# Kernel tuning notes

Hardware: AMD Instinct MI355X
Metric: run time of the kernel (lower is better)

Reference implementation:

```python
import jax, jax.numpy as jnp
import numpy as np

B, T, D, H = 8, 4096, 512, 64

def setup_inputs() -> dict:
    key = jax.random.key(0)
    ks = jax.random.split(key, 6)
    s = 0.02  # small init scale so exp(K), exp(wbias) stay numerically tame
    return {
        "x": jax.random.normal(ks[0], (B, T, D), dtype=jnp.float32),
        "wq": jax.random.normal(ks[1], (H, D), dtype=jnp.float32) * s,
        "bq": jnp.zeros((H,), dtype=jnp.float32),
        "wk": jax.random.normal(ks[2], (H, D), dtype=jnp.float32) * s,
        "bk": jnp.zeros((H,), dtype=jnp.float32),
        "wv": jax.random.normal(ks[3], (H, D), dtype=jnp.float32) * s,
        "bv": jnp.zeros((H,), dtype=jnp.float32),
        "wp": jax.random.normal(ks[4], (D, H), dtype=jnp.float32) * s,
        "bp": jnp.zeros((D,), dtype=jnp.float32),
        "wbias": jax.random.normal(ks[5], (T, T), dtype=jnp.float32) * s,
    }

def reference(x, wq, bq, wk, bk, wv, bv, wp, bp, wbias):
    # Q, K, V projections: [B, T, H]
    Q = jnp.einsum('btd,hd->bth', x, wq) + bq
    K = jnp.einsum('btd,hd->bth', x, wk) + bk
    V = jnp.einsum('btd,hd->bth', x, wv) + bv
    ew = jnp.exp(wbias)              # [T, T], computed once
    eK = jnp.exp(K)                  # [B, T, H]
    num = jnp.einsum('ts,bsh->bth', ew, eK * V)
    den = jnp.einsum('ts,bsh->bth', ew, eK)
    Yt = jax.nn.sigmoid(Q) * (num / den)
    # output projection back to dim: [B, T, D]
    return jnp.einsum('bth,dh->btd', Yt, wp) + bp
```

## Files before the change

kernel.cpp:

```cpp
#include <hip/hip_runtime.h>
#include <math.h>

typedef _Float16 f16;
typedef __attribute__((ext_vector_type(8))) _Float16 f16x8;
typedef __attribute__((ext_vector_type(4))) _Float16 f16x4;
typedef __attribute__((ext_vector_type(4))) float f32x4;
typedef __attribute__((ext_vector_type(16))) float f32x16;

#define MFMA16(a, b, c) __builtin_amdgcn_mfma_f32_16x16x32_f16((a), (b), (c), 0, 0, 0)
#define MFMA32(a, b, c) __builtin_amdgcn_mfma_f32_32x32x16_f16((a), (b), (c), 0, 0, 0)

__device__ __forceinline__ void gld16(const f16* g, f16* l) {
  __builtin_amdgcn_global_load_lds(
      (const __attribute__((address_space(1))) unsigned int*)g,
      (__attribute__((address_space(3))) unsigned int*)l, 16, 0, 0);
}

__device__ __forceinline__ f16x8 pack8(const float* src) {
  float4 f0 = *(const float4*)src;
  float4 f1 = *(const float4*)(src + 4);
  f16x8 v;
  v[0] = (f16)f0.x; v[1] = (f16)f0.y; v[2] = (f16)f0.z; v[3] = (f16)f0.w;
  v[4] = (f16)f1.x; v[5] = (f16)f1.y; v[6] = (f16)f1.z; v[7] = (f16)f1.w;
  return v;
}

__global__ __launch_bounds__(256) void prep_ew(const float* __restrict__ wb,
                                               f16* __restrict__ ew) {
  const size_t stride = (size_t)gridDim.x * 256;
  const size_t total = (size_t)4096 * 4096 / 4;
  for (size_t i = (size_t)blockIdx.x * 256 + threadIdx.x; i < total; i += stride) {
    float4 f = ((const float4*)wb)[i];
    f16x4 o;
    o.x = (f16)expf(f.x); o.y = (f16)expf(f.y);
    o.z = (f16)expf(f.z); o.w = (f16)expf(f.w);
    ((f16x4*)ew)[i] = o;
  }
}

__global__ __launch_bounds__(256) void prep_w(const float* __restrict__ wq,
                                              const float* __restrict__ wk,
                                              const float* __restrict__ wv,
                                              const float* __restrict__ wp,
                                              f16* __restrict__ wqkvb,
                                              f16* __restrict__ wpb) {
  int i = blockIdx.x * 256 + threadIdx.x;
  wqkvb[i] = (f16)wk[i];
  wqkvb[32768 + i] = (f16)wv[i];
  wqkvb[65536 + i] = (f16)wq[i];
  wpb[i] = (f16)wp[i];
}

__global__ __launch_bounds__(256) void k1_qkv(const float* __restrict__ x,
                                              const f16* __restrict__ wqkvb,
                                              const float* __restrict__ bq,
                                              const float* __restrict__ bk,
                                              const float* __restrict__ bv,
                                              f16* __restrict__ sigQ,
                                              f16* __restrict__ XT) {
  __shared__ alignas(16) f16 sW[192 * 64];
  __shared__ alignas(16) f16 sX[64 * 64];
  const int tid = threadIdx.x;
  const int wave = tid >> 6, lane = tid & 63;
  const int m0 = blockIdx.x * 64;
  const int l15 = lane & 15;

  f32x4 accQ[4], accK[4], accV[4];
#pragma unroll
  for (int j = 0; j < 4; ++j) {
    accQ[j] = (f32x4){0.f, 0.f, 0.f, 0.f};
    accK[j] = (f32x4){0.f, 0.f, 0.f, 0.f};
    accV[j] = (f32x4){0.f, 0.f, 0.f, 0.f};
  }

  const int sc8 = tid & 7;
  const int wr8 = (tid >> 3) & 7;
  const int wcol = (sc8 ^ wr8) * 8;

  for (int ks = 0; ks < 512; ks += 64) {
#pragma unroll
    for (int q = 0; q < 6; ++q) {
      int r = q * 32 + (tid >> 3);
      gld16(wqkvb + (size_t)r * 512 + ks + wcol, &sW[r * 64 + sc8 * 8]);
    }
#pragma unroll
    for (int u = 0; u < 2; ++u) {
      int un = tid + u * 256;
      int r = un >> 3, c8 = un & 7;
      *(f16x8*)&sX[r * 64 + ((c8 ^ (r & 7)) * 8)] =
          pack8(x + (size_t)(m0 + r) * 512 + ks + c8 * 8);
    }
    __syncthreads();
#pragma unroll
    for (int kk = 0; kk < 2; ++kk) {
      const int c = kk * 4 + (lane >> 4);
      const int rK = wave * 16 + l15;
      const int rV = 64 + rK;
      f16x8 aK = *(const f16x8*)&sW[rK * 64 + ((c ^ (rK & 7)) * 8)];
      f16x8 aV = *(const f16x8*)&sW[rV * 64 + ((c ^ (rV & 7)) * 8)];
      f16x8 aQ = *(const f16x8*)&sX[rK * 64 + ((c ^ (rK & 7)) * 8)];
#pragma unroll
      for (int j = 0; j < 4; ++j) {
        const int rX = j * 16 + l15;
        const int rWq = 128 + j * 16 + l15;
        f16x8 bx = *(const f16x8*)&sX[rX * 64 + ((c ^ (rX & 7)) * 8)];
        f16x8 bw = *(const f16x8*)&sW[rWq * 64 + ((c ^ (rWq & 7)) * 8)];
        accK[j] = MFMA16(aK, bx, accK[j]);
        accV[j] = MFMA16(aV, bx, accV[j]);
        accQ[j] = MFMA16(aQ, bw, accQ[j]);
      }
    }
    __syncthreads();
  }
  const int b = m0 >> 12, t0 = m0 & 4095;
#pragma unroll
  for (int j = 0; j < 4; ++j) {
    const int h = j * 16 + l15;
    const float bqv = bq[h];
#pragma unroll
    for (int r = 0; r < 4; ++r) {
      const int m = m0 + wave * 16 + (lane >> 4) * 4 + r;
      const float v = accQ[j][r] + bqv;
      sigQ[(size_t)m * 64 + h] = (f16)(1.f / (1.f + expf(-v)));
    }
  }
#pragma unroll
  for (int r = 0; r < 4; ++r) {
    const int h = wave * 16 + (lane >> 4) * 4 + r;
    const float bkv = bk[h], bvv = bv[h];
    const size_t rowKV = (size_t)(b * 128 + h) * 4096;
    const size_t rowK = (size_t)(b * 128 + 64 + h) * 4096;
#pragma unroll
    for (int j = 0; j < 4; ++j) {
      const int t = t0 + j * 16 + l15;
      const float ek = expf(accK[j][r] + bkv);
      const float ev = accV[j][r] + bvv;
      XT[rowKV + t] = (f16)(ek * ev);
      XT[rowK + t] = (f16)ek;
    }
  }
}

__global__ __launch_bounds__(512, 2) void k2_big(const f16* __restrict__ A,
                                                 const f16* __restrict__ Bm,
                                                 const f16* __restrict__ sigQ,
                                                 f16* __restrict__ Yt) {
  __shared__ alignas(16) f16 smem[4][128 * 128];
  const int tid = threadIdx.x;
  const int wave = tid >> 6, lane = tid & 63;
  const int kq = wave >> 1;
  const int ws = wave & 1;
  const int bid = blockIdx.x;
  const int b = (bid >> 3) & 7;
  const int m0 = ((bid & 7) + 8 * (bid >> 6)) * 128;
  const f16* Bbase = Bm + (size_t)(b * 128) * 4096;

  const int srow = tid >> 4;
  const int sc16 = tid & 15;
  const int gcol = (sc16 ^ (srow & 15)) * 8;

  f32x16 acc[4][2];
#pragma unroll
  for (int i = 0; i < 4; ++i)
#pragma unroll
    for (int j = 0; j < 2; ++j)
#pragma unroll
      for (int r = 0; r < 16; ++r) acc[i][j][r] = 0.f;

#define K2_STAGE(buf, ks)                                                          \
  do {                                                                             \
    _Pragma("unroll") for (int q = 0; q < 4; ++q) {                                \
      int r = q * 32 + srow;                                                       \
      gld16(A + (size_t)(m0 + r) * 4096 + (ks) + gcol,                             \
            &smem[buf][r * 128 + sc16 * 8]);                                       \
      gld16(Bbase + (size_t)r * 4096 + (ks) + gcol,                                \
            &smem[2 + (buf)][r * 128 + sc16 * 8]);                                 \
    }                                                                              \
  } while (0)

  K2_STAGE(0, 0);
  K2_STAGE(1, 128);
  asm volatile("s_waitcnt vmcnt(8)" ::: "memory");
  __builtin_amdgcn_s_barrier();
  asm volatile("" ::: "memory");

  const int l31 = lane & 31, l15 = lane & 15, lhi = lane >> 5;
  const int c0 = kq * 4 + lhi;
  const int cx0 = (c0 ^ l15) * 8;
  const int cx1 = ((c0 + 2) ^ l15) * 8;
  const int nk = 4096 / 128;
  for (int t = 0; t < nk; ++t) {
    const int buf = t & 1;
    const f16* pA = smem[buf];
    const f16* pB = smem[2 + buf];
    f16x8 a0[4], a1[4], b0[2], b1[2];
#pragma unroll
    for (int i = 0; i < 4; ++i) a0[i] = *(const f16x8*)&pA[(i * 32 + l31) * 128 + cx0];
#pragma unroll
    for (int j = 0; j < 2; ++j)
      b0[j] = *(const f16x8*)&pB[(j * 64 + ws * 32 + l31) * 128 + cx0];
#pragma unroll
    for (int i = 0; i < 4; ++i) a1[i] = *(const f16x8*)&pA[(i * 32 + l31) * 128 + cx1];
#pragma unroll
    for (int j = 0; j < 2; ++j)
      b1[j] = *(const f16x8*)&pB[(j * 64 + ws * 32 + l31) * 128 + cx1];
    __builtin_amdgcn_s_setprio(1);
#pragma unroll
    for (int i = 0; i < 4; ++i)
#pragma unroll
      for (int j = 0; j < 2; ++j) acc[i][j] = MFMA32(a0[i], b0[j], acc[i][j]);
#pragma unroll
    for (int i = 0; i < 4; ++i)
#pragma unroll
      for (int j = 0; j < 2; ++j) acc[i][j] = MFMA32(a1[i], b1[j], acc[i][j]);
    __builtin_amdgcn_s_setprio(0);
    if (t + 1 < nk) {
      asm volatile("s_waitcnt lgkmcnt(0)" ::: "memory");
      __builtin_amdgcn_s_barrier();
      asm volatile("" ::: "memory");
      if (t + 2 < nk) {
        K2_STAGE(buf, (t + 2) * 128);
        asm volatile("s_waitcnt vmcnt(8)" ::: "memory");
      } else {
        asm volatile("s_waitcnt vmcnt(0)" ::: "memory");
      }
      __builtin_amdgcn_s_barrier();
      asm volatile("" ::: "memory");
    }
  }
#undef K2_STAGE

  __syncthreads();
  float* scr = (float*)smem;
  const int rit0 = 4 * lhi;
#define MRG_ADDR(reg, i, j, r) \
  ((reg) * 16384 + ((i) * 32 + ((r) & 3) + 8 * ((r) >> 2) + rit0) * 128 + (j) * 64 + ws * 32 + l31)
  if (kq & 1) {
#pragma unroll
    for (int i = 0; i < 4; ++i)
#pragma unroll
      for (int j = 0; j < 2; ++j)
#pragma unroll
        for (int r = 0; r < 16; ++r) scr[MRG_ADDR(kq >> 1, i, j, r)] = acc[i][j][r];
  }
  __syncthreads();
  if (!(kq & 1)) {
#pragma unroll
    for (int i = 0; i < 4; ++i)
#pragma unroll
      for (int j = 0; j < 2; ++j)
#pragma unroll
        for (int r = 0; r < 16; ++r) acc[i][j][r] += scr[MRG_ADDR(kq >> 1, i, j, r)];
  }
  __syncthreads();
  if (kq == 2) {
#pragma unroll
    for (int i = 0; i < 4; ++i)
#pragma unroll
      for (int j = 0; j < 2; ++j)
#pragma unroll
        for (int r = 0; r < 16; ++r) scr[MRG_ADDR(0, i, j, r)] = acc[i][j][r];
  }
  __syncthreads();
  if (kq == 0) {
#pragma unroll
    for (int i = 0; i < 4; ++i)
#pragma unroll
      for (int j = 0; j < 2; ++j)
#pragma unroll
        for (int r = 0; r < 16; ++r) acc[i][j][r] += scr[MRG_ADDR(0, i, j, r)];
    const int h = ws * 32 + l31;
#pragma unroll
    for (int i = 0; i < 4; ++i)
#pragma unroll
      for (int r = 0; r < 16; ++r) {
        const int trow = m0 + i * 32 + (r & 3) + 8 * (r >> 2) + rit0;
        const size_t mrow = (size_t)b * 4096 + trow;
        const float sq = (float)sigQ[mrow * 64 + h];
        Yt[mrow * 64 + h] = (f16)(sq * acc[i][0][r] / acc[i][1][r]);
      }
  }
#undef MRG_ADDR
}

__global__ __launch_bounds__(256) void k4_out(const f16* __restrict__ Yt,
                                              const f16* __restrict__ wpb,
                                              const float* __restrict__ bp,
                                              float* __restrict__ out) {
  __shared__ alignas(16) f16 sA[128 * 64];
  __shared__ alignas(16) f16 sB[128 * 64];
  const int tid = threadIdx.x;
  const int wave = tid >> 6, lane = tid & 63;
  const int m0 = blockIdx.x * 128;
  const int n0 = blockIdx.y * 128;
  const int wm = (wave >> 1) * 64;
  const int wn = (wave & 1) * 64;
  const int l15 = lane & 15;
  const int sc8 = tid & 7;
  const int scol = (sc8 ^ ((tid >> 3) & 7)) * 8;

#pragma unroll
  for (int q = 0; q < 4; ++q) {
    int r = q * 32 + (tid >> 3);
    gld16(Yt + (size_t)(m0 + r) * 64 + scol, &sA[r * 64 + sc8 * 8]);
    gld16(wpb + (size_t)(n0 + r) * 64 + scol, &sB[r * 64 + sc8 * 8]);
  }
  __syncthreads();

  f32x4 acc[4][4];
#pragma unroll
  for (int i = 0; i < 4; ++i)
#pragma unroll
    for (int j = 0; j < 4; ++j) acc[i][j] = (f32x4){0.f, 0.f, 0.f, 0.f};

#pragma unroll
  for (int kk = 0; kk < 2; ++kk) {
    const int c = kk * 4 + (lane >> 4);
    f16x8 af[4], bfr[4];
#pragma unroll
    for (int i = 0; i < 4; ++i) {
      const int r = wm + i * 16 + l15;
      af[i] = *(const f16x8*)&sA[r * 64 + ((c ^ (r & 7)) * 8)];
    }
#pragma unroll
    for (int j = 0; j < 4; ++j) {
      const int r = wn + j * 16 + l15;
      bfr[j] = *(const f16x8*)&sB[r * 64 + ((c ^ (r & 7)) * 8)];
    }
#pragma unroll
    for (int i = 0; i < 4; ++i)
#pragma unroll
      for (int j = 0; j < 4; ++j) acc[i][j] = MFMA16(af[i], bfr[j], acc[i][j]);
  }

#pragma unroll
  for (int i = 0; i < 4; ++i) {
    const int row = m0 + wm + i * 16 + (lane >> 4) * 4;
#pragma unroll
    for (int j = 0; j < 4; ++j) {
      const int col = n0 + wn + j * 16 + l15;
      const float bpv = bp[col];
#pragma unroll
      for (int r = 0; r < 4; ++r)
        out[(size_t)(row + r) * 512 + col] = acc[i][j][r] + bpv;
    }
  }
}

extern "C" void kernel_launch(void* const* d_in, const int* in_sizes, int n_in,
                              void* d_out, int out_size, void* d_ws, size_t ws_size,
                              hipStream_t stream) {
  const float* x = (const float*)d_in[0];
  const float* wq = (const float*)d_in[1];
  const float* bq = (const float*)d_in[2];
  const float* wk = (const float*)d_in[3];
  const float* bk = (const float*)d_in[4];
  const float* wv = (const float*)d_in[5];
  const float* bv = (const float*)d_in[6];
  const float* wp = (const float*)d_in[7];
  const float* bp = (const float*)d_in[8];
  const float* wbias = (const float*)d_in[9];
  float* out = (float*)d_out;

  char* ws = (char*)d_ws;
  f16* ew = (f16*)(ws);
  f16* XT = (f16*)(ws + 33554432);
  f16* sigQ = (f16*)(ws + 41943040);
  f16* Yt = (f16*)(ws + 46137344);
  f16* wqkvb = (f16*)(ws + 50331648);
  f16* wpb = (f16*)(ws + 50528256);

  prep_ew<<<4096, 256, 0, stream>>>(wbias, ew);
  prep_w<<<128, 256, 0, stream>>>(wq, wk, wv, wp, wqkvb, wpb);
  k1_qkv<<<512, 256, 0, stream>>>(x, wqkvb, bq, bk, bv, sigQ, XT);
  k2_big<<<256, 512, 0, stream>>>(ew, XT, sigQ, Yt);
  k4_out<<<dim3(256, 4), 256, 0, stream>>>(Yt, wpb, bp, out);
}
```

Baseline: 99.63 us.

## Switch k2 to triple-buffered 64-wide K stages with single barrier per step

The main big GEMM kernel now uses a 3-stage ring of 64-column K tiles (96KB LDS) instead of double-buffered 128-column tiles (128KB). The next-next stage is issued at the start of each iteration, so there is one barrier per step instead of two. The cross-wave reduction is serialized to fit the smaller scratch area. Dropping the occupancy hint of 2 blocks per CU and halving K per step doubles the loop trips and barriers, which may reduce MFMA density per sync.

Result: no change. 99.33 us (-0.3%).

```diff
diff --git a/kernel.cpp b/kernel.cpp
--- a/kernel.cpp
+++ b/kernel.cpp
@@ -141,11 +141,11 @@
   }
 }
 
-__global__ __launch_bounds__(512, 2) void k2_big(const f16* __restrict__ A,
-                                                 const f16* __restrict__ Bm,
-                                                 const f16* __restrict__ sigQ,
-                                                 f16* __restrict__ Yt) {
-  __shared__ alignas(16) f16 smem[4][128 * 128];
+__global__ __launch_bounds__(512) void k2_big(const f16* __restrict__ A,
+                                              const f16* __restrict__ Bm,
+                                              const f16* __restrict__ sigQ,
+                                              f16* __restrict__ Yt) {
+  __shared__ alignas(16) f16 smem[3 * 16384];
   const int tid = threadIdx.x;
   const int wave = tid >> 6, lane = tid & 63;
   const int kq = wave >> 1;
@@ -153,11 +153,12 @@
   const int bid = blockIdx.x;
   const int b = (bid >> 3) & 7;
   const int m0 = ((bid & 7) + 8 * (bid >> 6)) * 128;
-  const f16* Bbase = Bm + (size_t)(b * 128) * 4096;
-
-  const int srow = tid >> 4;
-  const int sc16 = tid & 15;
-  const int gcol = (sc16 ^ (srow & 15)) * 8;
+  const f16* Bb = Bm + (size_t)(b * 128) * 4096;
+
+  const int srow8 = tid >> 3;
+  const int sc8 = tid & 7;
+  const int gsw = (sc8 ^ (srow8 & 7)) * 8;
+  const int dlin = srow8 * 64 + sc8 * 8;
 
   f32x16 acc[4][2];
 #pragma unroll
@@ -167,90 +168,88 @@
 #pragma unroll
       for (int r = 0; r < 16; ++r) acc[i][j][r] = 0.f;
 
-#define K2_STAGE(buf, ks)                                                          \
-  do {                                                                             \
-    _Pragma("unroll") for (int q = 0; q < 4; ++q) {                                \
-      int r = q * 32 + srow;                                                       \
-      gld16(A + (size_t)(m0 + r) * 4096 + (ks) + gcol,                             \
-            &smem[buf][r * 128 + sc16 * 8]);                                       \
-      gld16(Bbase + (size_t)r * 4096 + (ks) + gcol,                                \
-            &smem[2 + (buf)][r * 128 + sc16 * 8]);                                 \
-    }                                                                              \
+#define K2_STAGE(bb, ks)                                                         \
+  do {                                                                           \
+    gld16(A + (size_t)(m0 + srow8) * 4096 + (ks) + gsw, &smem[(bb) + dlin]);     \
+    gld16(A + (size_t)(m0 + 64 + srow8) * 4096 + (ks) + gsw,                     \
+          &smem[(bb) + 4096 + dlin]);                                            \
+    gld16(Bb + (size_t)srow8 * 4096 + (ks) + gsw, &smem[(bb) + 8192 + dlin]);    \
+    gld16(Bb + (size_t)(64 + srow8) * 4096 + (ks) + gsw,                         \
+          &smem[(bb) + 12288 + dlin]);                                           \
   } while (0)
 
   K2_STAGE(0, 0);
-  K2_STAGE(1, 128);
-  asm volatile("s_waitcnt vmcnt(8)" ::: "memory");
+  K2_STAGE(16384, 64);
+  asm volatile("s_waitcnt vmcnt(4)" ::: "memory");
+  __builtin_amdgcn_sched_barrier(0);
   __builtin_amdgcn_s_barrier();
-  asm volatile("" ::: "memory");
-
-  const int l31 = lane & 31, l15 = lane & 15, lhi = lane >> 5;
-  const int c0 = kq * 4 + lhi;
-  const int cx0 = (c0 ^ l15) * 8;
-  const int cx1 = ((c0 + 2) ^ l15) * 8;
-  const int nk = 4096 / 128;
+
+  const int l31 = lane & 31, lhi = lane >> 5;
+  const int cx = ((kq * 2 + lhi) ^ (lane & 7)) * 8;
+  const int nk = 64;
+  int bb = 0;
   for (int t = 0; t < nk; ++t) {
-    const int buf = t & 1;
-    const f16* pA = smem[buf];
-    const f16* pB = smem[2 + buf];
-    f16x8 a0[4], a1[4], b0[2], b1[2];
-#pragma unroll
-    for (int i = 0; i < 4; ++i) a0[i] = *(const f16x8*)&pA[(i * 32 + l31) * 128 + cx0];
+    int bb2 = bb + 32768;
+    if (bb2 >= 49152) bb2 -= 49152;
+    if (t < nk - 2) K2_STAGE(bb2, (t + 2) * 64);
+    const f16* pA = &smem[bb];
+    const f16* pB = &smem[bb + 8192];
+    f16x8 af[4], bf2[2];
+#pragma unroll
+    for (int i = 0; i < 4; ++i) af[i] = *(const f16x8*)&pA[(i * 32 + l31) * 64 + cx];
 #pragma unroll
     for (int j = 0; j < 2; ++j)
-      b0[j] = *(const f16x8*)&pB[(j * 64 + ws * 32 + l31) * 128 + cx0];
-#pragma unroll
-    for (int i = 0; i < 4; ++i) a1[i] = *(const f16x8*)&pA[(i * 32 + l31) * 128 + cx1];
-#pragma unroll
-    for (int j = 0; j < 2; ++j)
-      b1[j] = *(const f16x8*)&pB[(j * 64 + ws * 32 + l31) * 128 + cx1];
+      bf2[j] = *(const f16x8*)&pB[(j * 64 + ws * 32 + l31) * 64 + cx];
+    asm volatile("s_waitcnt lgkmcnt(0)" ::: "memory");
+    __builtin_amdgcn_sched_barrier(0);
     __builtin_amdgcn_s_setprio(1);
 #pragma unroll
     for (int i = 0; i < 4; ++i)
 #pragma unroll
-      for (int j = 0; j < 2; ++j) acc[i][j] = MFMA32(a0[i], b0[j], acc[i][j]);
-#pragma unroll
-    for (int i = 0; i < 4; ++i)
-#pragma unroll
-      for (int j = 0; j < 2; ++j) acc[i][j] = MFMA32(a1[i], b1[j], acc[i][j]);
+      for (int j = 0; j < 2; ++j) acc[i][j] = MFMA32(af[i], bf2[j], acc[i][j]);
     __builtin_amdgcn_s_setprio(0);
-    if (t + 1 < nk) {
-      asm volatile("s_waitcnt lgkmcnt(0)" ::: "memory");
-      __builtin_amdgcn_s_barrier();
-      asm volatile("" ::: "memory");
-      if (t + 2 < nk) {
-        K2_STAGE(buf, (t + 2) * 128);
-        asm volatile("s_waitcnt vmcnt(8)" ::: "memory");
-      } else {
-        asm volatile("s_waitcnt vmcnt(0)" ::: "memory");
-      }
-      __builtin_amdgcn_s_barrier();
-      asm volatile("" ::: "memory");
-    }
+    if (t < nk - 2) {
+      asm volatile("s_waitcnt vmcnt(4)" ::: "memory");
+    } else {
+      asm volatile("s_waitcnt vmcnt(0)" ::: "memory");
+    }
+    __builtin_amdgcn_sched_barrier(0);
+    __builtin_amdgcn_s_barrier();
+    bb += 16384;
+    if (bb == 49152) bb = 0;
   }
 #undef K2_STAGE
 
   __syncthreads();
   float* scr = (float*)smem;
   const int rit0 = 4 * lhi;
-#define MRG_ADDR(reg, i, j, r) \
-  ((reg) * 16384 + ((i) * 32 + ((r) & 3) + 8 * ((r) >> 2) + rit0) * 128 + (j) * 64 + ws * 32 + l31)
-  if (kq & 1) {
-#pragma unroll
-    for (int i = 0; i < 4; ++i)
-#pragma unroll
-      for (int j = 0; j < 2; ++j)
-#pragma unroll
-        for (int r = 0; r < 16; ++r) scr[MRG_ADDR(kq >> 1, i, j, r)] = acc[i][j][r];
-  }
-  __syncthreads();
-  if (!(kq & 1)) {
-#pragma unroll
-    for (int i = 0; i < 4; ++i)
-#pragma unroll
-      for (int j = 0; j < 2; ++j)
-#pragma unroll
-        for (int r = 0; r < 16; ++r) acc[i][j][r] += scr[MRG_ADDR(kq >> 1, i, j, r)];
+#define MRG(i, j, r) \
+  (((i) * 32 + ((r) & 3) + 8 * ((r) >> 2) + rit0) * 128 + (j) * 64 + ws * 32 + l31)
+  if (kq == 1) {
+#pragma unroll
+    for (int i = 0; i < 4; ++i)
+#pragma unroll
+      for (int j = 0; j < 2; ++j)
+#pragma unroll
+        for (int r = 0; r < 16; ++r) scr[MRG(i, j, r)] = acc[i][j][r];
+  }
+  __syncthreads();
+  if (kq == 0) {
+#pragma unroll
+    for (int i = 0; i < 4; ++i)
+#pragma unroll
+      for (int j = 0; j < 2; ++j)
+#pragma unroll
+        for (int r = 0; r < 16; ++r) acc[i][j][r] += scr[MRG(i, j, r)];
+  }
+  __syncthreads();
+  if (kq == 3) {
+#pragma unroll
+    for (int i = 0; i < 4; ++i)
+#pragma unroll
+      for (int j = 0; j < 2; ++j)
+#pragma unroll
+        for (int r = 0; r < 16; ++r) scr[MRG(i, j, r)] = acc[i][j][r];
   }
   __syncthreads();
   if (kq == 2) {
@@ -259,7 +258,16 @@
 #pragma unroll
       for (int j = 0; j < 2; ++j)
 #pragma unroll
-        for (int r = 0; r < 16; ++r) scr[MRG_ADDR(0, i, j, r)] = acc[i][j][r];
+        for (int r = 0; r < 16; ++r) acc[i][j][r] += scr[MRG(i, j, r)];
+  }
+  __syncthreads();
+  if (kq == 2) {
+#pragma unroll
+    for (int i = 0; i < 4; ++i)
+#pragma unroll
+      for (int j = 0; j < 2; ++j)
+#pragma unroll
+        for (int r = 0; r < 16; ++r) scr[MRG(i, j, r)] = acc[i][j][r];
   }
   __syncthreads();
   if (kq == 0) {
@@ -268,7 +276,7 @@
 #pragma unroll
       for (int j = 0; j < 2; ++j)
 #pragma unroll
-        for (int r = 0; r < 16; ++r) acc[i][j][r] += scr[MRG_ADDR(0, i, j, r)];
+        for (int r = 0; r < 16; ++r) acc[i][j][r] += scr[MRG(i, j, r)];
     const int h = ws * 32 + l31;
 #pragma unroll
     for (int i = 0; i < 4; ++i)
@@ -280,7 +288,7 @@
         Yt[mrow * 64 + h] = (f16)(sq * acc[i][0][r] / acc[i][1][r]);
       }
   }
-#undef MRG_ADDR
+#undef MRG
 }
 
 __global__ __launch_bounds__(256) void k4_out(const f16* __restrict__ Yt,
```

## Stage A tiles through registers with deeper prefetch in k2_big main loop

Applied to the files above, without the earlier changes.

The A operand of the big time-mixing GEMM is now loaded from global memory into registers three tiles ahead and then written to LDS. B keeps using direct global-to-LDS loads two tiles ahead. The loop is manually unrolled with ping-pong register buffers and sched_barriers, and explicit per-iteration vmcnt waits are dropped. The min-blocks-per-CU hint is removed, so the compiler gets more registers for the extra prefetch buffers. This aims to hide global latency better, at the cost of more VGPRs and relying on implicit waitcnt ordering for the asynchronous B loads.

Result: slower. 106.1 us (+6.5%).

```diff
diff --git a/kernel.cpp b/kernel.cpp
--- a/kernel.cpp
+++ b/kernel.cpp
@@ -141,11 +141,11 @@
   }
 }
 
-__global__ __launch_bounds__(512, 2) void k2_big(const f16* __restrict__ A,
-                                                 const f16* __restrict__ Bm,
-                                                 const f16* __restrict__ sigQ,
-                                                 f16* __restrict__ Yt) {
-  __shared__ alignas(16) f16 smem[4][128 * 128];
+__global__ __launch_bounds__(512) void k2_big(const f16* __restrict__ A,
+                                              const f16* __restrict__ Bm,
+                                              const f16* __restrict__ sigQ,
+                                              f16* __restrict__ Yt) {
+  __shared__ alignas(16) f16 smem[4][16384];
   const int tid = threadIdx.x;
   const int wave = tid >> 6, lane = tid & 63;
   const int kq = wave >> 1;
@@ -153,12 +153,20 @@
   const int bid = blockIdx.x;
   const int b = (bid >> 3) & 7;
   const int m0 = ((bid & 7) + 8 * (bid >> 6)) * 128;
-  const f16* Bbase = Bm + (size_t)(b * 128) * 4096;
+  const f16* Bb = Bm + (size_t)(b * 128) * 4096;
 
   const int srow = tid >> 4;
   const int sc16 = tid & 15;
   const int gcol = (sc16 ^ (srow & 15)) * 8;
 
+  int aRow[4], aCol[4];
+#pragma unroll
+  for (int u = 0; u < 4; ++u) {
+    int d = u * 512 + tid;
+    aRow[u] = d >> 4;
+    aCol[u] = ((d & 15) ^ ((d >> 4) & 15)) * 8;
+  }
+
   f32x16 acc[4][2];
 #pragma unroll
   for (int i = 0; i < 4; ++i)
@@ -167,68 +175,107 @@
 #pragma unroll
       for (int r = 0; r < 16; ++r) acc[i][j][r] = 0.f;
 
-#define K2_STAGE(buf, ks)                                                          \
-  do {                                                                             \
-    _Pragma("unroll") for (int q = 0; q < 4; ++q) {                                \
-      int r = q * 32 + srow;                                                       \
-      gld16(A + (size_t)(m0 + r) * 4096 + (ks) + gcol,                             \
-            &smem[buf][r * 128 + sc16 * 8]);                                       \
-      gld16(Bbase + (size_t)r * 4096 + (ks) + gcol,                                \
-            &smem[2 + (buf)][r * 128 + sc16 * 8]);                                 \
-    }                                                                              \
-  } while (0)
-
-  K2_STAGE(0, 0);
-  K2_STAGE(1, 128);
-  asm volatile("s_waitcnt vmcnt(8)" ::: "memory");
-  __builtin_amdgcn_s_barrier();
-  asm volatile("" ::: "memory");
+  f16x8 arE[4], arO[4];
 
   const int l31 = lane & 31, l15 = lane & 15, lhi = lane >> 5;
   const int c0 = kq * 4 + lhi;
   const int cx0 = (c0 ^ l15) * 8;
   const int cx1 = ((c0 + 2) ^ l15) * 8;
-  const int nk = 4096 / 128;
-  for (int t = 0; t < nk; ++t) {
-    const int buf = t & 1;
-    const f16* pA = smem[buf];
-    const f16* pB = smem[2 + buf];
-    f16x8 a0[4], a1[4], b0[2], b1[2];
-#pragma unroll
-    for (int i = 0; i < 4; ++i) a0[i] = *(const f16x8*)&pA[(i * 32 + l31) * 128 + cx0];
-#pragma unroll
-    for (int j = 0; j < 2; ++j)
-      b0[j] = *(const f16x8*)&pB[(j * 64 + ws * 32 + l31) * 128 + cx0];
-#pragma unroll
-    for (int i = 0; i < 4; ++i) a1[i] = *(const f16x8*)&pA[(i * 32 + l31) * 128 + cx1];
-#pragma unroll
-    for (int j = 0; j < 2; ++j)
-      b1[j] = *(const f16x8*)&pB[(j * 64 + ws * 32 + l31) * 128 + cx1];
-    __builtin_amdgcn_s_setprio(1);
-#pragma unroll
-    for (int i = 0; i < 4; ++i)
-#pragma unroll
-      for (int j = 0; j < 2; ++j) acc[i][j] = MFMA32(a0[i], b0[j], acc[i][j]);
-#pragma unroll
-    for (int i = 0; i < 4; ++i)
-#pragma unroll
-      for (int j = 0; j < 2; ++j) acc[i][j] = MFMA32(a1[i], b1[j], acc[i][j]);
-    __builtin_amdgcn_s_setprio(0);
-    if (t + 1 < nk) {
-      asm volatile("s_waitcnt lgkmcnt(0)" ::: "memory");
-      __builtin_amdgcn_s_barrier();
-      asm volatile("" ::: "memory");
-      if (t + 2 < nk) {
-        K2_STAGE(buf, (t + 2) * 128);
-        asm volatile("s_waitcnt vmcnt(8)" ::: "memory");
-      } else {
-        asm volatile("s_waitcnt vmcnt(0)" ::: "memory");
-      }
-      __builtin_amdgcn_s_barrier();
-      asm volatile("" ::: "memory");
-    }
-  }
-#undef K2_STAGE
+
+#define SB0 __builtin_amdgcn_sched_barrier(0)
+
+#define K2_ALOAD(dst, T)                                                        \
+  do {                                                                          \
+    _Pragma("unroll") for (int u = 0; u < 4; ++u)                               \
+        dst[u] = *(const f16x8*)(A + (size_t)(m0 + aRow[u]) * 4096 +            \
+                                 (size_t)(T) * 128 + aCol[u]);                  \
+  } while (0)
+
+#define K2_AWRITE(c, src)                                                       \
+  do {                                                                          \
+    _Pragma("unroll") for (int u = 0; u < 4; ++u)                               \
+        *(f16x8*)&smem[c][(u * 512 + tid) * 8] = src[u];                        \
+  } while (0)
+
+#define K2_BSTAGE(c, T)                                                         \
+  do {                                                                          \
+    _Pragma("unroll") for (int q = 0; q < 4; ++q) {                             \
+      int r = q * 32 + srow;                                                    \
+      gld16(Bb + (size_t)r * 4096 + (size_t)(T) * 128 + gcol,                   \
+            &smem[2 + (c)][r * 128 + sc16 * 8]);                                \
+    }                                                                           \
+  } while (0)
+
+#define K2_COMPUTE(c)                                                           \
+  do {                                                                          \
+    const f16* pA = smem[c];                                                    \
+    const f16* pB = smem[2 + (c)];                                              \
+    f16x8 a0[4], a1[4], b0[2], b1[2];                                           \
+    _Pragma("unroll") for (int i = 0; i < 4; ++i)                               \
+        a0[i] = *(const f16x8*)&pA[(i * 32 + l31) * 128 + cx0];                 \
+    _Pragma("unroll") for (int j = 0; j < 2; ++j)                               \
+        b0[j] = *(const f16x8*)&pB[(j * 64 + ws * 32 + l31) * 128 + cx0];       \
+    _Pragma("unroll") for (int i = 0; i < 4; ++i)                               \
+        a1[i] = *(const f16x8*)&pA[(i * 32 + l31) * 128 + cx1];                 \
+    _Pragma("unroll") for (int j = 0; j < 2; ++j)                               \
+        b1[j] = *(const f16x8*)&pB[(j * 64 + ws * 32 + l31) * 128 + cx1];       \
+    __builtin_amdgcn_s_setprio(1);                                              \
+    _Pragma("unroll") for (int i = 0; i < 4; ++i)                               \
+        _Pragma("unroll") for (int j = 0; j < 2; ++j)                           \
+            acc[i][j] = MFMA32(a0[i], b0[j], acc[i][j]);                        \
+    _Pragma("unroll") for (int i = 0; i < 4; ++i)                               \
+        _Pragma("unroll") for (int j = 0; j < 2; ++j)                           \
+            acc[i][j] = MFMA32(a1[i], b1[j], acc[i][j]);                        \
+    __builtin_amdgcn_s_setprio(0);                                              \
+  } while (0)
+
+#define K2_BODY(T, CUR, NXT, DOLOAD)                                            \
+  do {                                                                          \
+    K2_COMPUTE((T) & 1);                                                        \
+    SB0;                                                                        \
+    __builtin_amdgcn_s_barrier();                                               \
+    SB0;                                                                        \
+    K2_AWRITE((T) & 1, CUR);   \
+    K2_BSTAGE((T) & 1, (T) + 2);                                                \
+    if (DOLOAD) K2_ALOAD(NXT, (T) + 3);                                         \
+    asm volatile("s_waitcnt lgkmcnt(0)" ::: "memory");                          \
+    SB0;                                                                        \
+    __builtin_amdgcn_s_barrier();                                               \
+    SB0;                                                                        \
+  } while (0)
+
+  K2_ALOAD(arE, 0);
+  K2_BSTAGE(0, 0);
+  K2_AWRITE(0, arE);
+  K2_ALOAD(arO, 1);
+  K2_BSTAGE(1, 1);
+  K2_AWRITE(1, arO);
+  K2_ALOAD(arE, 2);
+  asm volatile("s_waitcnt lgkmcnt(0)" ::: "memory");
+  SB0;
+  __builtin_amdgcn_s_barrier();
+  SB0;
+
+  for (int t = 0; t < 28; t += 2) {
+    K2_BODY(t, arE, arO, 1);
+    K2_BODY(t + 1, arO, arE, 1);
+  }
+  K2_BODY(28, arE, arO, 1);
+  K2_BODY(29, arO, arE, 0);
+  K2_COMPUTE(0);
+  SB0;
+  __builtin_amdgcn_s_barrier();
+  SB0;
+  asm volatile("s_waitcnt vmcnt(0)" ::: "memory");
+  SB0;
+  __builtin_amdgcn_s_barrier();
+  SB0;
+  K2_COMPUTE(1);
+#undef K2_BODY
+#undef K2_COMPUTE
+#undef K2_BSTAGE
+#undef K2_AWRITE
+#undef K2_ALOAD
 
   __syncthreads();
   float* scr = (float*)smem;
@@ -281,6 +328,7 @@
       }
   }
 #undef MRG_ADDR
+#undef SB0
 }
 
 __global__ __launch_bounds__(256) void k4_out(const f16* __restrict__ Yt,
```

## Fuse output projection into big GEMM kernel, widen to 1024 threads, merge prep kernels

Applied to the files above, without the earlier changes.

Merges the two prep kernels into one launch and fuses the output projection (Yt·Wp^T + bp) into the epilogue of the main exp(wbias)×XT GEMM, so Yt is never written to or read back from global memory. The main kernel moves to 1024-thread blocks, giving each of 16 waves a 2x2 tile of 32x32 MFMAs with a 4-way split-K reduced through LDS. It also switches to sched_barrier fencing. The trade-offs are lower occupancy (one block per CU), a heavier epilogue, and fewer MFMAs per wave per LDS load in the main loop.

Measured after the change: 95.66 us. -4.0%, faster.

```diff
diff --git a/kernel.cpp b/kernel.cpp
--- a/kernel.cpp
+++ b/kernel.cpp
@@ -25,8 +25,14 @@
   return v;
 }
 
-__global__ __launch_bounds__(256) void prep_ew(const float* __restrict__ wb,
-                                               f16* __restrict__ ew) {
+__global__ __launch_bounds__(256) void prep_ewpw(const float* __restrict__ wb,
+                                                 f16* __restrict__ ew,
+                                                 const float* __restrict__ wq,
+                                                 const float* __restrict__ wk,
+                                                 const float* __restrict__ wv,
+                                                 const float* __restrict__ wp,
+                                                 f16* __restrict__ wqkvb,
+                                                 f16* __restrict__ wpb) {
   const size_t stride = (size_t)gridDim.x * 256;
   const size_t total = (size_t)4096 * 4096 / 4;
   for (size_t i = (size_t)blockIdx.x * 256 + threadIdx.x; i < total; i += stride) {
@@ -36,19 +42,13 @@
     o.z = (f16)expf(f.z); o.w = (f16)expf(f.w);
     ((f16x4*)ew)[i] = o;
   }
-}
-
-__global__ __launch_bounds__(256) void prep_w(const float* __restrict__ wq,
-                                              const float* __restrict__ wk,
-                                              const float* __restrict__ wv,
-                                              const float* __restrict__ wp,
-                                              f16* __restrict__ wqkvb,
-                                              f16* __restrict__ wpb) {
-  int i = blockIdx.x * 256 + threadIdx.x;
-  wqkvb[i] = (f16)wk[i];
-  wqkvb[32768 + i] = (f16)wv[i];
-  wqkvb[65536 + i] = (f16)wq[i];
-  wpb[i] = (f16)wp[i];
+  if (blockIdx.x < 128) {
+    int i = blockIdx.x * 256 + threadIdx.x;
+    wqkvb[i] = (f16)wk[i];
+    wqkvb[32768 + i] = (f16)wv[i];
+    wqkvb[65536 + i] = (f16)wq[i];
+    wpb[i] = (f16)wp[i];
+  }
 }
 
 __global__ __launch_bounds__(256) void k1_qkv(const float* __restrict__ x,
@@ -141,210 +141,216 @@
   }
 }
 
-__global__ __launch_bounds__(512, 2) void k2_big(const f16* __restrict__ A,
-                                                 const f16* __restrict__ Bm,
-                                                 const f16* __restrict__ sigQ,
-                                                 f16* __restrict__ Yt) {
-  __shared__ alignas(16) f16 smem[4][128 * 128];
+__global__ __launch_bounds__(1024) void k2_big(const f16* __restrict__ A,
+                                               const f16* __restrict__ Bm,
+                                               const f16* __restrict__ sigQ,
+                                               const f16* __restrict__ wpb,
+                                               const float* __restrict__ bp,
+                                               float* __restrict__ out) {
+  __shared__ alignas(16) f16 smem[4][16384];
   const int tid = threadIdx.x;
-  const int wave = tid >> 6, lane = tid & 63;
-  const int kq = wave >> 1;
-  const int ws = wave & 1;
+  const int w = tid >> 6, lane = tid & 63;
+  const int kq = w >> 2;
+  const int wr = (w >> 1) & 1;
+  const int wc = w & 1;
   const int bid = blockIdx.x;
   const int b = (bid >> 3) & 7;
   const int m0 = ((bid & 7) + 8 * (bid >> 6)) * 128;
-  const f16* Bbase = Bm + (size_t)(b * 128) * 4096;
-
-  const int srow = tid >> 4;
-  const int sc16 = tid & 15;
-  const int gcol = (sc16 ^ (srow & 15)) * 8;
-
-  f32x16 acc[4][2];
-#pragma unroll
-  for (int i = 0; i < 4; ++i)
+  const f16* Bb = Bm + (size_t)(b * 128) * 4096;
+
+  int sRow[2], sCol[2];
+#pragma unroll
+  for (int u = 0; u < 2; ++u) {
+    int d = u * 1024 + tid;
+    sRow[u] = d >> 4;
+    sCol[u] = ((d & 15) ^ ((d >> 4) & 15)) * 8;
+  }
+
+  f32x16 acc[2][2];
+#pragma unroll
+  for (int i = 0; i < 2; ++i)
 #pragma unroll
     for (int j = 0; j < 2; ++j)
 #pragma unroll
       for (int r = 0; r < 16; ++r) acc[i][j][r] = 0.f;
 
-#define K2_STAGE(buf, ks)                                                          \
-  do {                                                                             \
-    _Pragma("unroll") for (int q = 0; q < 4; ++q) {                                \
-      int r = q * 32 + srow;                                                       \
-      gld16(A + (size_t)(m0 + r) * 4096 + (ks) + gcol,                             \
-            &smem[buf][r * 128 + sc16 * 8]);                                       \
-      gld16(Bbase + (size_t)r * 4096 + (ks) + gcol,                                \
-            &smem[2 + (buf)][r * 128 + sc16 * 8]);                                 \
-    }                                                                              \
+#define SB0 __builtin_amdgcn_sched_barrier(0)
+#define K2_STAGE(buf, ks)                                                       \
+  do {                                                                          \
+    _Pragma("unroll") for (int u = 0; u < 2; ++u) {                             \
+      gld16(A + (size_t)(m0 + sRow[u]) * 4096 + (ks) + sCol[u],                 \
+            &smem[buf][(u * 1024 + tid) * 8]);                                  \
+      gld16(Bb + (size_t)sRow[u] * 4096 + (ks) + sCol[u],                       \
+            &smem[2 + (buf)][(u * 1024 + tid) * 8]);                            \
+    }                                                                           \
   } while (0)
 
   K2_STAGE(0, 0);
   K2_STAGE(1, 128);
-  asm volatile("s_waitcnt vmcnt(8)" ::: "memory");
+  asm volatile("s_waitcnt vmcnt(4)" ::: "memory");
+  SB0;
   __builtin_amdgcn_s_barrier();
-  asm volatile("" ::: "memory");
+  SB0;
 
   const int l31 = lane & 31, l15 = lane & 15, lhi = lane >> 5;
   const int c0 = kq * 4 + lhi;
   const int cx0 = (c0 ^ l15) * 8;
   const int cx1 = ((c0 + 2) ^ l15) * 8;
-  const int nk = 4096 / 128;
+  const int arow0 = (wr * 64 + l31) * 128;
+  const int arow1 = (wr * 64 + 32 + l31) * 128;
+  const int brow0 = (wc * 32 + l31) * 128;
+  const int brow1 = (64 + wc * 32 + l31) * 128;
+
+  const int nk = 32;
   for (int t = 0; t < nk; ++t) {
-    const int buf = t & 1;
-    const f16* pA = smem[buf];
-    const f16* pB = smem[2 + buf];
-    f16x8 a0[4], a1[4], b0[2], b1[2];
-#pragma unroll
-    for (int i = 0; i < 4; ++i) a0[i] = *(const f16x8*)&pA[(i * 32 + l31) * 128 + cx0];
-#pragma unroll
-    for (int j = 0; j < 2; ++j)
-      b0[j] = *(const f16x8*)&pB[(j * 64 + ws * 32 + l31) * 128 + cx0];
-#pragma unroll
-    for (int i = 0; i < 4; ++i) a1[i] = *(const f16x8*)&pA[(i * 32 + l31) * 128 + cx1];
-#pragma unroll
-    for (int j = 0; j < 2; ++j)
-      b1[j] = *(const f16x8*)&pB[(j * 64 + ws * 32 + l31) * 128 + cx1];
+    const int cur = t & 1;
+    const f16* pA = smem[cur];
+    const f16* pB = smem[2 + cur];
+    f16x8 a00 = *(const f16x8*)&pA[arow0 + cx0];
+    f16x8 a10 = *(const f16x8*)&pA[arow1 + cx0];
+    f16x8 b00 = *(const f16x8*)&pB[brow0 + cx0];
+    f16x8 b10 = *(const f16x8*)&pB[brow1 + cx0];
+    f16x8 a01 = *(const f16x8*)&pA[arow0 + cx1];
+    f16x8 a11 = *(const f16x8*)&pA[arow1 + cx1];
+    f16x8 b01 = *(const f16x8*)&pB[brow0 + cx1];
+    f16x8 b11 = *(const f16x8*)&pB[brow1 + cx1];
     __builtin_amdgcn_s_setprio(1);
-#pragma unroll
-    for (int i = 0; i < 4; ++i)
-#pragma unroll
-      for (int j = 0; j < 2; ++j) acc[i][j] = MFMA32(a0[i], b0[j], acc[i][j]);
-#pragma unroll
-    for (int i = 0; i < 4; ++i)
-#pragma unroll
-      for (int j = 0; j < 2; ++j) acc[i][j] = MFMA32(a1[i], b1[j], acc[i][j]);
+    acc[0][0] = MFMA32(a00, b00, acc[0][0]);
+    acc[0][1] = MFMA32(a00, b10, acc[0][1]);
+    acc[1][0] = MFMA32(a10, b00, acc[1][0]);
+    acc[1][1] = MFMA32(a10, b10, acc[1][1]);
+    acc[0][0] = MFMA32(a01, b01, acc[0][0]);
+    acc[0][1] = MFMA32(a01, b11, acc[0][1]);
+    acc[1][0] = MFMA32(a11, b01, acc[1][0]);
+    acc[1][1] = MFMA32(a11, b11, acc[1][1]);
     __builtin_amdgcn_s_setprio(0);
-    if (t + 1 < nk) {
-      asm volatile("s_waitcnt lgkmcnt(0)" ::: "memory");
-      __builtin_amdgcn_s_barrier();
-      asm volatile("" ::: "memory");
-      if (t + 2 < nk) {
-        K2_STAGE(buf, (t + 2) * 128);
-        asm volatile("s_waitcnt vmcnt(8)" ::: "memory");
-      } else {
-        asm volatile("s_waitcnt vmcnt(0)" ::: "memory");
+    asm volatile("s_waitcnt lgkmcnt(0)" ::: "memory");
+    SB0;
+    __builtin_amdgcn_s_barrier();
+    SB0;
+    if (t + 2 < nk) {
+      K2_STAGE(cur, (t + 2) * 128);
+      asm volatile("s_waitcnt vmcnt(4)" ::: "memory");
+    } else {
+      asm volatile("s_waitcnt vmcnt(0)" ::: "memory");
+    }
+    SB0;
+    __builtin_amdgcn_s_barrier();
+    SB0;
+  }
+#undef K2_STAGE
+
+  f16x8 wpr[4];
+#pragma unroll
+  for (int u = 0; u < 4; ++u)
+    wpr[u] = *(const f16x8*)(wpb + (size_t)(u * 1024 + tid) * 8);
+
+  __syncthreads();
+  float* scr = (float*)smem;
+#define MADDR(reg, i, j, r) \
+  ((reg) * 16384 + (((wr * 2 + wc) * 4 + (i) * 2 + (j)) << 10) + ((r) << 6) + lane)
+  if (kq == 1) {
+#pragma unroll
+    for (int i = 0; i < 2; ++i)
+#pragma unroll
+      for (int j = 0; j < 2; ++j)
+#pragma unroll
+        for (int r = 0; r < 16; ++r) scr[MADDR(0, i, j, r)] = acc[i][j][r];
+  }
+  if (kq == 3) {
+#pragma unroll
+    for (int i = 0; i < 2; ++i)
+#pragma unroll
+      for (int j = 0; j < 2; ++j)
+#pragma unroll
+        for (int r = 0; r < 16; ++r) scr[MADDR(1, i, j, r)] = acc[i][j][r];
+  }
+  __syncthreads();
+  if (kq == 0) {
+#pragma unroll
+    for (int i = 0; i < 2; ++i)
+#pragma unroll
+      for (int j = 0; j < 2; ++j)
+#pragma unroll
+        for (int r = 0; r < 16; ++r) acc[i][j][r] += scr[MADDR(0, i, j, r)];
+  }
+  if (kq == 2) {
+#pragma unroll
+    for (int i = 0; i < 2; ++i)
+#pragma unroll
+      for (int j = 0; j < 2; ++j)
+#pragma unroll
+        for (int r = 0; r < 16; ++r) acc[i][j][r] += scr[MADDR(1, i, j, r)];
+  }
+  __syncthreads();
+  if (kq == 2) {
+#pragma unroll
+    for (int i = 0; i < 2; ++i)
+#pragma unroll
+      for (int j = 0; j < 2; ++j)
+#pragma unroll
+        for (int r = 0; r < 16; ++r) scr[MADDR(0, i, j, r)] = acc[i][j][r];
+  }
+  __syncthreads();
+  if (kq == 0) {
+#pragma unroll
+    for (int i = 0; i < 2; ++i)
+#pragma unroll
+      for (int j = 0; j < 2; ++j)
+#pragma unroll
+        for (int r = 0; r < 16; ++r) acc[i][j][r] += scr[MADDR(0, i, j, r)];
+  }
+#undef MADDR
+  __syncthreads();
+
+  f16* sYt = (f16*)smem;
+  f16* sWp = (f16*)smem + 9216;
+  if (kq == 0) {
+#pragma unroll
+    for (int i = 0; i < 2; ++i)
+#pragma unroll
+      for (int r = 0; r < 16; ++r) {
+        const int trow = wr * 64 + i * 32 + (r & 3) + 8 * (r >> 2) + 4 * lhi;
+        const int h = wc * 32 + l31;
+        const size_t mrow = (size_t)b * 4096 + m0 + trow;
+        const float sq = (float)sigQ[mrow * 64 + h];
+        sYt[trow * 68 + h] = (f16)(sq * acc[i][0][r] / acc[i][1][r]);
       }
-      __builtin_amdgcn_s_barrier();
-      asm volatile("" ::: "memory");
-    }
-  }
-#undef K2_STAGE
-
-  __syncthreads();
-  float* scr = (float*)smem;
-  const int rit0 = 4 * lhi;
-#define MRG_ADDR(reg, i, j, r) \
-  ((reg) * 16384 + ((i) * 32 + ((r) & 3) + 8 * ((r) >> 2) + rit0) * 128 + (j) * 64 + ws * 32 + l31)
-  if (kq & 1) {
-#pragma unroll
-    for (int i = 0; i < 4; ++i)
-#pragma unroll
-      for (int j = 0; j < 2; ++j)
-#pragma unroll
-        for (int r = 0; r < 16; ++r) scr[MRG_ADDR(kq >> 1, i, j, r)] = acc[i][j][r];
-  }
-  __syncthreads();
-  if (!(kq & 1)) {
-#pragma unroll
-    for (int i = 0; i < 4; ++i)
-#pragma unroll
-      for (int j = 0; j < 2; ++j)
-#pragma unroll
-        for (int r = 0; r < 16; ++r) acc[i][j][r] += scr[MRG_ADDR(kq >> 1, i, j, r)];
-  }
-  __syncthreads();
-  if (kq == 2) {
-#pragma unroll
-    for (int i = 0; i < 4; ++i)
-#pragma unroll
-      for (int j = 0; j < 2; ++j)
-#pragma unroll
-        for (int r = 0; r < 16; ++r) scr[MRG_ADDR(0, i, j, r)] = acc[i][j][r];
-  }
-  __syncthreads();
-  if (kq == 0) {
-#pragma unroll
-    for (int i = 0; i < 4; ++i)
-#pragma unroll
-      for (int j = 0; j < 2; ++j)
-#pragma unroll
-        for (int r = 0; r < 16; ++r) acc[i][j][r] += scr[MRG_ADDR(0, i, j, r)];
-    const int h = ws * 32 + l31;
-#pragma unroll
-    for (int i = 0; i < 4; ++i)
-#pragma unroll
-      for (int r = 0; r < 16; ++r) {
-        const int trow = m0 + i * 32 + (r & 3) + 8 * (r >> 2) + rit0;
-        const size_t mrow = (size_t)b * 4096 + trow;
-        const float sq = (float)sigQ[mrow * 64 + h];
-        Yt[mrow * 64 + h] = (f16)(sq * acc[i][0][r] / acc[i][1][r]);
-      }
-  }
-#undef MRG_ADDR
-}
-
-__global__ __launch_bounds__(256) void k4_out(const f16* __restrict__ Yt,
-                                              const f16* __restrict__ wpb,
-                                              const float* __restrict__ bp,
-                                              float* __restrict__ out) {
-  __shared__ alignas(16) f16 sA[128 * 64];
-  __shared__ alignas(16) f16 sB[128 * 64];
-  const int tid = threadIdx.x;
-  const int wave = tid >> 6, lane = tid & 63;
-  const int m0 = blockIdx.x * 128;
-  const int n0 = blockIdx.y * 128;
-  const int wm = (wave >> 1) * 64;
-  const int wn = (wave & 1) * 64;
-  const int l15 = lane & 15;
-  const int sc8 = tid & 7;
-  const int scol = (sc8 ^ ((tid >> 3) & 7)) * 8;
-
-#pragma unroll
-  for (int q = 0; q < 4; ++q) {
-    int r = q * 32 + (tid >> 3);
-    gld16(Yt + (size_t)(m0 + r) * 64 + scol, &sA[r * 64 + sc8 * 8]);
-    gld16(wpb + (size_t)(n0 + r) * 64 + scol, &sB[r * 64 + sc8 * 8]);
-  }
-  __syncthreads();
-
-  f32x4 acc[4][4];
-#pragma unroll
-  for (int i = 0; i < 4; ++i)
-#pragma unroll
-    for (int j = 0; j < 4; ++j) acc[i][j] = (f32x4){0.f, 0.f, 0.f, 0.f};
-
-#pragma unroll
-  for (int kk = 0; kk < 2; ++kk) {
-    const int c = kk * 4 + (lane >> 4);
-    f16x8 af[4], bfr[4];
-#pragma unroll
-    for (int i = 0; i < 4; ++i) {
-      const int r = wm + i * 16 + l15;
-      af[i] = *(const f16x8*)&sA[r * 64 + ((c ^ (r & 7)) * 8)];
-    }
-#pragma unroll
-    for (int j = 0; j < 4; ++j) {
-      const int r = wn + j * 16 + l15;
-      bfr[j] = *(const f16x8*)&sB[r * 64 + ((c ^ (r & 7)) * 8)];
-    }
-#pragma unroll
-    for (int i = 0; i < 4; ++i)
-#pragma unroll
-      for (int j = 0; j < 4; ++j) acc[i][j] = MFMA16(af[i], bfr[j], acc[i][j]);
-  }
-
-#pragma unroll
-  for (int i = 0; i < 4; ++i) {
-    const int row = m0 + wm + i * 16 + (lane >> 4) * 4;
-#pragma unroll
-    for (int j = 0; j < 4; ++j) {
-      const int col = n0 + wn + j * 16 + l15;
-      const float bpv = bp[col];
-#pragma unroll
-      for (int r = 0; r < 4; ++r)
-        out[(size_t)(row + r) * 512 + col] = acc[i][j][r] + bpv;
-    }
-  }
+  }
+#pragma unroll
+  for (int u = 0; u < 4; ++u) {
+    const int d = u * 1024 + tid;
+    *(f16x8*)&sWp[(d >> 3) * 68 + (d & 7) * 8] = wpr[u];
+  }
+  __syncthreads();
+
+  f32x16 oacc[4];
+#pragma unroll
+  for (int cb = 0; cb < 4; ++cb)
+#pragma unroll
+    for (int r = 0; r < 16; ++r) oacc[cb][r] = 0.f;
+  const int yrow = (w & 3) * 32 + l31;
+  const int dbase = (w >> 2) * 128;
+#pragma unroll
+  for (int c = 0; c < 4; ++c) {
+    f16x8 ay = *(const f16x8*)&sYt[yrow * 68 + c * 16 + lhi * 8];
+#pragma unroll
+    for (int cb = 0; cb < 4; ++cb) {
+      f16x8 bw = *(const f16x8*)&sWp[(dbase + cb * 32 + l31) * 68 + c * 16 + lhi * 8];
+      oacc[cb] = MFMA32(ay, bw, oacc[cb]);
+    }
+  }
+#pragma unroll
+  for (int cb = 0; cb < 4; ++cb) {
+    const int od = dbase + cb * 32 + l31;
+    const float bpv = bp[od];
+#pragma unroll
+    for (int r = 0; r < 16; ++r) {
+      const int orow = (w & 3) * 32 + (r & 3) + 8 * (r >> 2) + 4 * lhi;
+      out[((size_t)(b * 4096 + m0 + orow)) * 512 + od] = oacc[cb][r] + bpv;
+    }
+  }
+#undef SB0
 }
 
 extern "C" void kernel_launch(void* const* d_in, const int* in_sizes, int n_in,
@@ -366,13 +372,10 @@
   f16* ew = (f16*)(ws);
   f16* XT = (f16*)(ws + 33554432);
   f16* sigQ = (f16*)(ws + 41943040);
-  f16* Yt = (f16*)(ws + 46137344);
-  f16* wqkvb = (f16*)(ws + 50331648);
-  f16* wpb = (f16*)(ws + 50528256);
-
-  prep_ew<<<4096, 256, 0, stream>>>(wbias, ew);
-  prep_w<<<128, 256, 0, stream>>>(wq, wk, wv, wp, wqkvb, wpb);
+  f16* wqkvb = (f16*)(ws + 46137344);
+  f16* wpb = (f16*)(ws + 46333952);
+
+  prep_ewpw<<<4096, 256, 0, stream>>>(wbias, ew, wq, wk, wv, wp, wqkvb, wpb);
   k1_qkv<<<512, 256, 0, stream>>>(x, wqkvb, bq, bk, bv, sigQ, XT);
-  k2_big<<<256, 512, 0, stream>>>(ew, XT, sigQ, Yt);
-  k4_out<<<dim3(256, 4), 256, 0, stream>>>(Yt, wpb, bp, out);
-}
+  k2_big<<<256, 1024, 0, stream>>>(ew, XT, sigQ, wpb, bp, out);
+}
```
